# Performance work log

Hardware: AMD Instinct MI355X
Metric: run time of the kernel (lower is better)

Reference implementation:

```python
import jax, jax.numpy as jnp
import numpy as np

N_NODES = 100000
N_EDGES = 1600000
D = 128
N_LAYERS = 3
N_GRAPHS = 128


def setup_inputs() -> dict:
    key = jax.random.key(0)
    ks = jax.random.split(key, 8)
    x = jax.random.normal(ks[0], (N_NODES, D), dtype=jnp.float32)
    # stacked GIN-MLP params (all layers are D->D since hidden_dim == in_dim)
    scale = 1.0 / np.sqrt(D)
    W1 = jax.random.normal(ks[1], (N_LAYERS, D, D), dtype=jnp.float32) * scale
    b1 = jax.random.normal(ks[2], (N_LAYERS, D), dtype=jnp.float32) * 0.01
    W2 = jax.random.normal(ks[3], (N_LAYERS, D, D), dtype=jnp.float32) * scale
    b2 = jax.random.normal(ks[4], (N_LAYERS, D), dtype=jnp.float32) * 0.01
    edge_index = jax.random.randint(ks[5], (2, N_EDGES), 0, N_NODES, dtype=jnp.int64)
    batch = jnp.sort(jax.random.randint(ks[6], (N_NODES,), 0, N_GRAPHS, dtype=jnp.int64))
    return {"x": x, "W1": W1, "b1": b1, "W2": W2, "b2": b2,
            "edge_index": edge_index, "batch": batch}


def reference(x, W1, b1, W2, b2, edge_index, batch):
    src = edge_index[0]
    dst = edge_index[1]
    n = x.shape[0]
    eps = jnp.float32(0.0)  # GIN eps (PyG default, not trained)
    for i in range(N_LAYERS):
        # gather neighbor features along edges, scatter-add to destination nodes
        agg = jax.ops.segment_sum(x[src], dst, num_segments=n)  # [N, D]
        h = (1.0 + eps) * x + agg
        h = jax.nn.relu(h @ W1[i] + b1[i])
        x = h @ W2[i] + b2[i]
    # sum-pool readout per graph
    h_G = jax.ops.segment_sum(x, batch, num_segments=N_GRAPHS)  # [G, D]
    return h_G
```

## Files before the change

kernel.cpp:

```cpp
#include <hip/hip_runtime.h>
#include <hip/hip_bf16.h>
#include <stdint.h>

#define N_NODES 100000
#define N_EDGES 1600000
#define DIM 128
#define N_GRAPHS 128
#define LDA 136

#define NBKT 392
#define BCAP 6144
#define BP   5632

#define NBIN_BLK 391
#define CVT_BLK 3125

typedef unsigned int uint32;
typedef unsigned short ushort16;

typedef __bf16 bf16x8 __attribute__((ext_vector_type(8)));
typedef float fx4 __attribute__((ext_vector_type(4)));

__device__ __forceinline__ float bfLo(uint32 u){ return __builtin_bit_cast(float, (uint32)(u << 16)); }
__device__ __forceinline__ float bfHi(uint32 u){ return __builtin_bit_cast(float, (uint32)(u & 0xFFFF0000u)); }
__device__ __forceinline__ ushort16 f2bf(float f){
  uint32 u = __builtin_bit_cast(uint32, f);
  u = u + 0x7FFFu + ((u >> 16) & 1u);
  return (ushort16)(u >> 16);
}
__device__ __forceinline__ uint32 pack2(float a, float b){
  return (uint32)f2bf(a) | ((uint32)f2bf(b) << 16);
}

__global__ __launch_bounds__(512) void k_prep(const float* __restrict__ x,
                                              const float* __restrict__ W1, const float* __restrict__ W2,
                                              const int* __restrict__ ei,
                                              ushort16* __restrict__ P, ushort16* __restrict__ Q,
                                              ushort16* __restrict__ Wf,
                                              int* __restrict__ bucketCursor,
                                              int* __restrict__ temp){
  __shared__ int hist[NBKT];
  __shared__ int base[NBKT];
  __shared__ int gbase[NBKT];
  __shared__ int scanbuf[512];
  __shared__ int sVal[4096];
  __shared__ unsigned short sBkt[4096];

  int bb = blockIdx.x;
  int t  = threadIdx.x;

  if (bb < NBIN_BLK){
    int e0 = bb * 4096;
    for (int i = t; i < NBKT; i += 512) hist[i] = 0;
    __syncthreads();

    int   myv[8];
    short myb[8];
    short myr[8];
    #pragma unroll
    for (int it = 0; it < 8; ++it){
      int e = e0 + it*512 + t;
      int v = 0; short b = -1; short r = 0;
      if (e < N_EDGES){
        int s = ei[e];
        int d = ei[N_EDGES + e];
        b = (short)(d >> 8);
        v = s | ((d & 255) << 17);
        r = (short)atomicAdd(&hist[b], 1);
      }
      myv[it] = v; myb[it] = b; myr[it] = r;
    }
    __syncthreads();

    scanbuf[t] = (t < NBKT) ? hist[t] : 0;
    __syncthreads();
    for (int off = 1; off < 512; off <<= 1){
      int x2 = 0;
      if (t >= off) x2 = scanbuf[t - off];
      __syncthreads();
      scanbuf[t] += x2;
      __syncthreads();
    }
    if (t < NBKT){
      base[t]  = scanbuf[t] - hist[t];
      gbase[t] = atomicAdd(&bucketCursor[t], hist[t]);
    }
    __syncthreads();

    #pragma unroll
    for (int it = 0; it < 8; ++it){
      if (myb[it] >= 0){
        int p = base[myb[it]] + myr[it];
        sVal[p] = myv[it];
        sBkt[p] = (unsigned short)myb[it];
      }
    }
    __syncthreads();

    int cnt = scanbuf[NBKT - 1];
    for (int p = t; p < cnt; p += 512){
      int b = sBkt[p];
      int g = gbase[b] + (p - base[b]);
      if (g < BCAP) temp[b*BCAP + g] = sVal[p];
    }
    return;
  }

  if (bb < NBIN_BLK + CVT_BLK){
    int idx = ((bb - NBIN_BLK)*512 + t) * 8;
    float4 v0 = *(const float4*)(x + idx);
    float4 v1 = *(const float4*)(x + idx + 4);
    uint4 o;
    o.x = pack2(v0.x, v0.y); o.y = pack2(v0.z, v0.w);
    o.z = pack2(v1.x, v1.y); o.w = pack2(v1.z, v1.w);
    *(uint4*)(P + idx) = o;
    return;
  }

  if (bb == NBIN_BLK + CVT_BLK){
    uint4 z = {0u,0u,0u,0u};
    if (t < 16)                *(uint4*)(P + (size_t)N_NODES*128 + t*8)      = z;
    else if (t < 32)           *(uint4*)(Q + (size_t)N_NODES*128 + (t-16)*8) = z;
    return;
  }

  int tid = (bb - (NBIN_BLK + CVT_BLK + 1))*512 + t;
  int layer = tid >> 12;
  int rem   = tid & 4095;
  int mat   = rem >> 11;
  int nt    = (rem >> 8) & 7;
  int kt    = (rem >> 6) & 3;
  int lane  = rem & 63;
  int kg = lane >> 4, m = lane & 15;
  int n  = nt*16 + m;
  int kb = kt*32 + kg*8;
  const float* src = (mat ? W2 : W1) + layer*16384;
  uint4 o;
  o.x = pack2(src[(kb+0)*128 + n], src[(kb+1)*128 + n]);
  o.y = pack2(src[(kb+2)*128 + n], src[(kb+3)*128 + n]);
  o.z = pack2(src[(kb+4)*128 + n], src[(kb+5)*128 + n]);
  o.w = pack2(src[(kb+6)*128 + n], src[(kb+7)*128 + n]);
  *(uint4*)(Wf + ((((size_t)(layer*2+mat)*8 + nt)*4 + kt)*64 + lane)*8) = o;
}

__global__ __launch_bounds__(512) void k_binB(const int* __restrict__ temp,
                                              const int* __restrict__ bucketCursor,
                                              int* __restrict__ rowptr,
                                              int* __restrict__ rowlen,
                                              int* __restrict__ colx){
  __shared__ int counts[256];
  __shared__ int sc[256];
  __shared__ int cur[256];
  __shared__ int stage[BCAP];
  __shared__ int sorted[BCAP];
  int b = blockIdx.x, t = threadIdx.x;
  int cnt = min(bucketCursor[b], BCAP);
  int gb  = b * BP;
  const int* src = temp + b*BCAP;

  if (t < 256) counts[t] = 0;
  __syncthreads();
  for (int p = t; p < cnt; p += 512){
    int v = src[p];
    stage[p] = v;
    atomicAdd(&counts[v >> 17], 1);
  }
  __syncthreads();

  int len = 0, plen = 0;
  if (t < 256){
    len  = counts[t];
    plen = (len + 3) & ~3;
    sc[t] = plen;
  }
  __syncthreads();
  for (int off = 1; off < 256; off <<= 1){
    int x = 0;
    if (t < 256 && t >= off) x = sc[t - off];
    __syncthreads();
    if (t < 256) sc[t] += x;
    __syncthreads();
  }
  int excl = 0;
  if (t < 256){
    excl = sc[t] - plen;
    cur[t] = excl;
    int node = b*256 + t;
    if (node < N_NODES){ rowptr[node] = gb + excl; rowlen[node] = plen; }
  }
  __syncthreads();

  for (int p = t; p < cnt; p += 512){
    int v = stage[p];
    int d = v >> 17;
    int pos = atomicAdd(&cur[d], 1);
    sorted[pos] = v & 0x1FFFF;
  }
  __syncthreads();

  if (t < 256){
    for (int k = len; k < plen; ++k) sorted[excl + k] = N_NODES;
  }
  __syncthreads();

  int total = min(sc[255], BP);
  for (int p = t; p < total; p += 512) colx[gb + p] = sorted[p];
}

__global__ __launch_bounds__(256, 8) void k_gin(const ushort16* __restrict__ xb, ushort16* __restrict__ hb,
                                                const ushort16* __restrict__ Wt1, const float* __restrict__ b1,
                                                const ushort16* __restrict__ Wt2, const float* __restrict__ b2,
                                                const int* __restrict__ rowptr, const int* __restrict__ rowlen,
                                                const int* __restrict__ colx){
  __shared__ __attribute__((aligned(16))) ushort16 sA[64 * LDA];
  __shared__ int sOff[64];
  __shared__ int sLen[64];

  int t = threadIdx.x;
  int row0 = blockIdx.x * 64;

  if (t < 64){
    int gg = row0 + t;
    int off = 0, len = 0;
    if (gg < N_NODES){ off = rowptr[gg]; len = rowlen[gg]; }
    sOff[t] = off; sLen[t] = len;
  }
  __syncthreads();

  int wave = t >> 6, lane = t & 63;
  int g = lane >> 4, o = lane & 15;
  const uint32* xw = (const uint32*)xb;

  for (int ni = 0; ni < 16; ++ni){
    int ln  = wave*16 + ni;
    int j   = __builtin_amdgcn_readfirstlane(sOff[ln]);
    int end = j + __builtin_amdgcn_readfirstlane(sLen[ln]);

    float f0=0.f,f1=0.f,f2=0.f,f3=0.f,f4=0.f,f5=0.f,f6=0.f,f7=0.f;

    while (j + 8 <= end){
      int4 c0 = *(const int4*)(colx + j);
      int4 c1 = *(const int4*)(colx + j + 4);
      int r0ab = (g & 1) ? c0.y : c0.x;
      int r0cd = (g & 1) ? c0.w : c0.z;
      int r0   = (g & 2) ? r0cd : r0ab;
      int r1ab = (g & 1) ? c1.y : c1.x;
      int r1cd = (g & 1) ? c1.w : c1.z;
      int r1   = (g & 2) ? r1cd : r1ab;
      uint4 u0 = *(const uint4*)(xw + (size_t)r0*64 + o*4);
      uint4 u1 = *(const uint4*)(xw + (size_t)r1*64 + o*4);
      f0 += bfLo(u0.x); f1 += bfHi(u0.x); f2 += bfLo(u0.y); f3 += bfHi(u0.y);
      f4 += bfLo(u0.z); f5 += bfHi(u0.z); f6 += bfLo(u0.w); f7 += bfHi(u0.w);
      f0 += bfLo(u1.x); f1 += bfHi(u1.x); f2 += bfLo(u1.y); f3 += bfHi(u1.y);
      f4 += bfLo(u1.z); f5 += bfHi(u1.z); f6 += bfLo(u1.w); f7 += bfHi(u1.w);
      j += 8;
    }
    if (j < end){
      int4 c0 = *(const int4*)(colx + j);
      int rab = (g & 1) ? c0.y : c0.x;
      int rcd = (g & 1) ? c0.w : c0.z;
      int r0  = (g & 2) ? rcd : rab;
      uint4 u0 = *(const uint4*)(xw + (size_t)r0*64 + o*4);
      f0 += bfLo(u0.x); f1 += bfHi(u0.x); f2 += bfLo(u0.y); f3 += bfHi(u0.y);
      f4 += bfLo(u0.z); f5 += bfHi(u0.z); f6 += bfLo(u0.w); f7 += bfHi(u0.w);
    }

    f0 += __shfl_xor(f0, 16, 64); f1 += __shfl_xor(f1, 16, 64);
    f2 += __shfl_xor(f2, 16, 64); f3 += __shfl_xor(f3, 16, 64);
    f4 += __shfl_xor(f4, 16, 64); f5 += __shfl_xor(f5, 16, 64);
    f6 += __shfl_xor(f6, 16, 64); f7 += __shfl_xor(f7, 16, 64);
    f0 += __shfl_xor(f0, 32, 64); f1 += __shfl_xor(f1, 32, 64);
    f2 += __shfl_xor(f2, 32, 64); f3 += __shfl_xor(f3, 32, 64);
    f4 += __shfl_xor(f4, 32, 64); f5 += __shfl_xor(f5, 32, 64);
    f6 += __shfl_xor(f6, 32, 64); f7 += __shfl_xor(f7, 32, 64);

    if (g == 0){
      int gn = row0 + ln;
      uint4 r;
      if (gn < N_NODES){
        uint4 xv = *(const uint4*)(xw + (size_t)gn*64 + o*4);
        r.x = pack2(f0 + bfLo(xv.x), f1 + bfHi(xv.x));
        r.y = pack2(f2 + bfLo(xv.y), f3 + bfHi(xv.y));
        r.z = pack2(f4 + bfLo(xv.z), f5 + bfHi(xv.z));
        r.w = pack2(f6 + bfLo(xv.w), f7 + bfHi(xv.w));
      } else {
        r.x = r.y = r.z = r.w = 0u;
      }
      *(uint4*)(sA + ln*LDA + o*8) = r;
    }
  }
  __syncthreads();

  int m = lane & 15, kg = lane >> 4;
  int n0 = wave * 2;

  fx4 acc[4][2];
  #pragma unroll
  for (int mt = 0; mt < 4; ++mt){ acc[mt][0] = (fx4){0,0,0,0}; acc[mt][1] = (fx4){0,0,0,0}; }

  #pragma unroll
  for (int kt = 0; kt < 4; ++kt){
    bf16x8 ba = *(const bf16x8*)(Wt1 + (((n0+0)*4 + kt)*64 + lane)*8);
    bf16x8 bb = *(const bf16x8*)(Wt1 + (((n0+1)*4 + kt)*64 + lane)*8);
    #pragma unroll
    for (int mt = 0; mt < 4; ++mt){
      bf16x8 av = *(const bf16x8*)(sA + (mt*16 + m)*LDA + kg*8 + kt*32);
      acc[mt][0] = __builtin_amdgcn_mfma_f32_16x16x32_bf16(av, ba, acc[mt][0], 0, 0, 0);
      acc[mt][1] = __builtin_amdgcn_mfma_f32_16x16x32_bf16(av, bb, acc[mt][1], 0, 0, 0);
    }
  }
  float bva = b1[(n0+0)*16 + m];
  float bvb = b1[(n0+1)*16 + m];
  __syncthreads();

  #pragma unroll
  for (int mt = 0; mt < 4; ++mt){
    #pragma unroll
    for (int r = 0; r < 4; ++r){
      int row = mt*16 + kg*4 + r;
      sA[row*LDA + (n0+0)*16 + m] = f2bf(fmaxf(acc[mt][0][r] + bva, 0.f));
      sA[row*LDA + (n0+1)*16 + m] = f2bf(fmaxf(acc[mt][1][r] + bvb, 0.f));
    }
  }
  float cva = b2[(n0+0)*16 + m];
  float cvb = b2[(n0+1)*16 + m];
  #pragma unroll
  for (int mt = 0; mt < 4; ++mt){ acc[mt][0] = (fx4){0,0,0,0}; acc[mt][1] = (fx4){0,0,0,0}; }
  __syncthreads();

  #pragma unroll
  for (int kt = 0; kt < 4; ++kt){
    bf16x8 ba = *(const bf16x8*)(Wt2 + (((n0+0)*4 + kt)*64 + lane)*8);
    bf16x8 bb = *(const bf16x8*)(Wt2 + (((n0+1)*4 + kt)*64 + lane)*8);
    #pragma unroll
    for (int mt = 0; mt < 4; ++mt){
      bf16x8 av = *(const bf16x8*)(sA + (mt*16 + m)*LDA + kg*8 + kt*32);
      acc[mt][0] = __builtin_amdgcn_mfma_f32_16x16x32_bf16(av, ba, acc[mt][0], 0, 0, 0);
      acc[mt][1] = __builtin_amdgcn_mfma_f32_16x16x32_bf16(av, bb, acc[mt][1], 0, 0, 0);
    }
  }

  #pragma unroll
  for (int mt = 0; mt < 4; ++mt){
    #pragma unroll
    for (int r = 0; r < 4; ++r){
      int row = row0 + mt*16 + kg*4 + r;
      if (row < N_NODES){
        hb[row*128 + (n0+0)*16 + m] = f2bf(acc[mt][0][r] + cva);
        hb[row*128 + (n0+1)*16 + m] = f2bf(acc[mt][1][r] + cvb);
      }
    }
  }
}

__device__ __forceinline__ int lower_bound_i(const int* __restrict__ a, int n, int key){
  int lo = 0, hi = n;
  while (lo < hi){ int mid = (lo + hi) >> 1; if (a[mid] < key) lo = mid + 1; else hi = mid; }
  return lo;
}

__global__ __launch_bounds__(256) void k_pool(const ushort16* __restrict__ xb, const int* __restrict__ batch,
                                              float* __restrict__ out){
  int g = blockIdx.x >> 2;
  int p = blockIdx.x & 3;
  int start = lower_bound_i(batch, N_NODES, g);
  int end   = lower_bound_i(batch, N_NODES, g + 1);
  int t = threadIdx.x;
  int c = t & 127;
  int h = t >> 7;
  float acc = 0.f;
  for (int r = start + p*2 + h; r < end; r += 8){
    uint32 u = (uint32)xb[r*128 + c];
    acc += __builtin_bit_cast(float, (uint32)(u << 16));
  }
  __shared__ float red[256];
  red[t] = acc; __syncthreads();
  if (t < 128) atomicAdd(&out[g*128 + c], red[t] + red[t + 128]);
}

extern "C" void kernel_launch(void* const* d_in, const int* in_sizes, int n_in,
                              void* d_out, int out_size, void* d_ws, size_t ws_size,
                              hipStream_t stream) {
  const float* x   = (const float*)d_in[0];
  const float* W1  = (const float*)d_in[1];
  const float* b1  = (const float*)d_in[2];
  const float* W2  = (const float*)d_in[3];
  const float* b2  = (const float*)d_in[4];
  const int*   ei  = (const int*)d_in[5];
  const int*   bat = (const int*)d_in[6];
  float* out = (float*)d_out;

  char* w = (char*)d_ws;
  auto carve = [&](size_t bytes) -> char* {
    char* p = w; w += (bytes + 255) & ~(size_t)255; return p;
  };
  ushort16* P    = (ushort16*)carve((size_t)(N_NODES+1) * DIM * 2);
  ushort16* Q    = (ushort16*)carve((size_t)(N_NODES+1) * DIM * 2);
  ushort16* Wf   = (ushort16*)carve((size_t)3 * 2 * 16384 * 2);
  int* rowptr    = (int*)carve((size_t)N_NODES * 4);
  int* rowlen    = (int*)carve((size_t)N_NODES * 4);
  int* colx      = (int*)carve((size_t)NBKT * BP * 4);
  int* bucketCursor = (int*)carve((NBKT + 1) * 4);
  int* temp      = (int*)Q;

  hipMemsetAsync(bucketCursor, 0, (NBKT + 1) * 4, stream);
  hipMemsetAsync(d_out, 0, (size_t)N_GRAPHS * DIM * 4, stream);

  k_prep<<<NBIN_BLK + CVT_BLK + 1 + 24, 512, 0, stream>>>(x, W1, W2, ei, P, Q, Wf,
                                                          bucketCursor, temp);
  k_binB<<<NBKT, 512, 0, stream>>>(temp, bucketCursor, rowptr, rowlen, colx);

  const int ginGrid = (N_NODES + 63) / 64;

  k_gin<<<ginGrid, 256, 0, stream>>>(P, Q, Wf + 0*16384, b1 + 0*128, Wf + 1*16384, b2 + 0*128,
                                     rowptr, rowlen, colx);
  k_gin<<<ginGrid, 256, 0, stream>>>(Q, P, Wf + 2*16384, b1 + 1*128, Wf + 3*16384, b2 + 1*128,
                                     rowptr, rowlen, colx);
  k_gin<<<ginGrid, 256, 0, stream>>>(P, Q, Wf + 4*16384, b1 + 2*128, Wf + 5*16384, b2 + 2*128,
                                     rowptr, rowlen, colx);

  k_pool<<<N_GRAPHS * 4, 256, 0, stream>>>(Q, bat, out);
}
```

Baseline: 362.9 us.

## Fuse sum-pool readout into last GIN layer and use 512-thread blocks

```diff
diff --git a/kernel.cpp b/kernel.cpp
--- a/kernel.cpp
+++ b/kernel.cpp
@@ -207,23 +207,29 @@
   for (int p = t; p < total; p += 512) colx[gb + p] = sorted[p];
 }
 
-__global__ __launch_bounds__(256, 8) void k_gin(const ushort16* __restrict__ xb, ushort16* __restrict__ hb,
+template<bool LAST>
+__global__ __launch_bounds__(512, 8) void k_gin(const ushort16* __restrict__ xb, ushort16* __restrict__ hb,
                                                 const ushort16* __restrict__ Wt1, const float* __restrict__ b1,
                                                 const ushort16* __restrict__ Wt2, const float* __restrict__ b2,
                                                 const int* __restrict__ rowptr, const int* __restrict__ rowlen,
-                                                const int* __restrict__ colx){
+                                                const int* __restrict__ colx,
+                                                const int* __restrict__ batch, float* __restrict__ outp){
   __shared__ __attribute__((aligned(16))) ushort16 sA[64 * LDA];
   __shared__ int sOff[64];
   __shared__ int sLen[64];
+  __shared__ int sBat[64];
 
   int t = threadIdx.x;
   int row0 = blockIdx.x * 64;
 
   if (t < 64){
     int gg = row0 + t;
-    int off = 0, len = 0;
-    if (gg < N_NODES){ off = rowptr[gg]; len = rowlen[gg]; }
-    sOff[t] = off; sLen[t] = len;
+    int off = 0, len = 0, bg = 0;
+    if (gg < N_NODES){
+      off = rowptr[gg]; len = rowlen[gg];
+      if (LAST) bg = batch[gg];
+    }
+    sOff[t] = off; sLen[t] = len; sBat[t] = bg;
   }
   __syncthreads();
 
@@ -231,8 +237,8 @@
   int g = lane >> 4, o = lane & 15;
   const uint32* xw = (const uint32*)xb;
 
-  for (int ni = 0; ni < 16; ++ni){
-    int ln  = wave*16 + ni;
+  for (int ni = 0; ni < 8; ++ni){
+    int ln  = wave*8 + ni;
     int j   = __builtin_amdgcn_readfirstlane(sOff[ln]);
     int end = j + __builtin_amdgcn_readfirstlane(sLen[ln]);
 
@@ -292,25 +298,22 @@
   __syncthreads();
 
   int m = lane & 15, kg = lane >> 4;
-  int n0 = wave * 2;
-
-  fx4 acc[4][2];
+  int nt = wave;
+
+  fx4 acc[4];
   #pragma unroll
-  for (int mt = 0; mt < 4; ++mt){ acc[mt][0] = (fx4){0,0,0,0}; acc[mt][1] = (fx4){0,0,0,0}; }
+  for (int mt = 0; mt < 4; ++mt) acc[mt] = (fx4){0.f,0.f,0.f,0.f};
 
   #pragma unroll
   for (int kt = 0; kt < 4; ++kt){
-    bf16x8 ba = *(const bf16x8*)(Wt1 + (((n0+0)*4 + kt)*64 + lane)*8);
-    bf16x8 bb = *(const bf16x8*)(Wt1 + (((n0+1)*4 + kt)*64 + lane)*8);
+    bf16x8 ba = *(const bf16x8*)(Wt1 + ((nt*4 + kt)*64 + lane)*8);
     #pragma unroll
     for (int mt = 0; mt < 4; ++mt){
       bf16x8 av = *(const bf16x8*)(sA + (mt*16 + m)*LDA + kg*8 + kt*32);
-      acc[mt][0] = __builtin_amdgcn_mfma_f32_16x16x32_bf16(av, ba, acc[mt][0], 0, 0, 0);
-      acc[mt][1] = __builtin_amdgcn_mfma_f32_16x16x32_bf16(av, bb, acc[mt][1], 0, 0, 0);
-    }
-  }
-  float bva = b1[(n0+0)*16 + m];
-  float bvb = b1[(n0+1)*16 + m];
+      acc[mt] = __builtin_amdgcn_mfma_f32_16x16x32_bf16(av, ba, acc[mt], 0, 0, 0);
+    }
+  }
+  float bva = b1[nt*16 + m];
   __syncthreads();
 
   #pragma unroll
@@ -318,64 +321,55 @@
     #pragma unroll
     for (int r = 0; r < 4; ++r){
       int row = mt*16 + kg*4 + r;
-      sA[row*LDA + (n0+0)*16 + m] = f2bf(fmaxf(acc[mt][0][r] + bva, 0.f));
-      sA[row*LDA + (n0+1)*16 + m] = f2bf(fmaxf(acc[mt][1][r] + bvb, 0.f));
-    }
-  }
-  float cva = b2[(n0+0)*16 + m];
-  float cvb = b2[(n0+1)*16 + m];
+      sA[row*LDA + nt*16 + m] = f2bf(fmaxf(acc[mt][r] + bva, 0.f));
+    }
+  }
+  float cva = b2[nt*16 + m];
   #pragma unroll
-  for (int mt = 0; mt < 4; ++mt){ acc[mt][0] = (fx4){0,0,0,0}; acc[mt][1] = (fx4){0,0,0,0}; }
+  for (int mt = 0; mt < 4; ++mt) acc[mt] = (fx4){0.f,0.f,0.f,0.f};
   __syncthreads();
 
   #pragma unroll
   for (int kt = 0; kt < 4; ++kt){
-    bf16x8 ba = *(const bf16x8*)(Wt2 + (((n0+0)*4 + kt)*64 + lane)*8);
-    bf16x8 bb = *(const bf16x8*)(Wt2 + (((n0+1)*4 + kt)*64 + lane)*8);
+    bf16x8 ba = *(const bf16x8*)(Wt2 + ((nt*4 + kt)*64 + lane)*8);
     #pragma unroll
     for (int mt = 0; mt < 4; ++mt){
       bf16x8 av = *(const bf16x8*)(sA + (mt*16 + m)*LDA + kg*8 + kt*32);
-      acc[mt][0] = __builtin_amdgcn_mfma_f32_16x16x32_bf16(av, ba, acc[mt][0], 0, 0, 0);
-      acc[mt][1] = __builtin_amdgcn_mfma_f32_16x16x32_bf16(av, bb, acc[mt][1], 0, 0, 0);
-    }
-  }
-
-  #pragma unroll
-  for (int mt = 0; mt < 4; ++mt){
-    #pragma unroll
-    for (int r = 0; r < 4; ++r){
-      int row = row0 + mt*16 + kg*4 + r;
-      if (row < N_NODES){
-        hb[row*128 + (n0+0)*16 + m] = f2bf(acc[mt][0][r] + cva);
-        hb[row*128 + (n0+1)*16 + m] = f2bf(acc[mt][1][r] + cvb);
+      acc[mt] = __builtin_amdgcn_mfma_f32_16x16x32_bf16(av, ba, acc[mt], 0, 0, 0);
+    }
+  }
+
+  if constexpr (!LAST){
+    #pragma unroll
+    for (int mt = 0; mt < 4; ++mt){
+      #pragma unroll
+      for (int r = 0; r < 4; ++r){
+        int row = row0 + mt*16 + kg*4 + r;
+        if (row < N_NODES){
+          hb[row*128 + nt*16 + m] = f2bf(acc[mt][r] + cva);
+        }
       }
     }
-  }
-}
-
-__device__ __forceinline__ int lower_bound_i(const int* __restrict__ a, int n, int key){
-  int lo = 0, hi = n;
-  while (lo < hi){ int mid = (lo + hi) >> 1; if (a[mid] < key) lo = mid + 1; else hi = mid; }
-  return lo;
-}
-
-__global__ __launch_bounds__(256) void k_pool(const ushort16* __restrict__ xb, const int* __restrict__ batch,
-                                              float* __restrict__ out){
-  int g = blockIdx.x >> 2;
-  int p = blockIdx.x & 3;
-  int start = lower_bound_i(batch, N_NODES, g);
-  int end   = lower_bound_i(batch, N_NODES, g + 1);
-  int t = threadIdx.x;
-  int c = t & 127;
-  int h = t >> 7;
-  float acc = 0.f;
-  for (int r = start + p*2 + h; r < end; r += 8){
-    uint32 u = (uint32)xb[r*128 + c];
-    acc += __builtin_bit_cast(float, (uint32)(u << 16));
-  }
-  __shared__ float red[256];
-  red[t] = acc; __syncthreads();
-  if (t < 128) atomicAdd(&out[g*128 + c], red[t] + red[t + 128]);
+  } else {
+    float sum = 0.f; int curg = -1;
+    #pragma unroll
+    for (int mt = 0; mt < 4; ++mt){
+      #pragma unroll
+      for (int r = 0; r < 4; ++r){
+        int lrow = mt*16 + kg*4 + r;
+        int grow = row0 + lrow;
+        if (grow < N_NODES){
+          int gg = sBat[lrow];
+          if (gg != curg){
+            if (curg >= 0) atomicAdd(&outp[curg*128 + nt*16 + m], sum);
+            curg = gg; sum = 0.f;
+          }
+          sum += acc[mt][r] + cva;
+        }
+      }
+    }
+    if (curg >= 0) atomicAdd(&outp[curg*128 + nt*16 + m], sum);
+  }
 }
 
 extern "C" void kernel_launch(void* const* d_in, const int* in_sizes, int n_in,
@@ -412,12 +406,10 @@
 
   const int ginGrid = (N_NODES + 63) / 64;
 
-  k_gin<<<ginGrid, 256, 0, stream>>>(P, Q, Wf + 0*16384, b1 + 0*128, Wf + 1*16384, b2 + 0*128,
-                                     rowptr, rowlen, colx);
-  k_gin<<<ginGrid, 256, 0, stream>>>(Q, P, Wf + 2*16384, b1 + 1*128, Wf + 3*16384, b2 + 1*128,
-                                     rowptr, rowlen, colx);
-  k_gin<<<ginGrid, 256, 0, stream>>>(P, Q, Wf + 4*16384, b1 + 2*128, Wf + 5*16384, b2 + 2*128,
-                                     rowptr, rowlen, colx);
-
-  k_pool<<<N_GRAPHS * 4, 256, 0, stream>>>(Q, bat, out);
-}
+  k_gin<false><<<ginGrid, 512, 0, stream>>>(P, Q, Wf + 0*16384, b1 + 0*128, Wf + 1*16384, b2 + 0*128,
+                                            rowptr, rowlen, colx, bat, out);
+  k_gin<false><<<ginGrid, 512, 0, stream>>>(Q, P, Wf + 2*16384, b1 + 1*128, Wf + 3*16384, b2 + 1*128,
+                                            rowptr, rowlen, colx, bat, out);
+  k_gin<true><<<ginGrid, 512, 0, stream>>>(P, Q, Wf + 4*16384, b1 + 2*128, Wf + 5*16384, b2 + 2*128,
+                                           rowptr, rowlen, colx, bat, out);
+}
```

Measured after the change: 329.9 us. 1.1x faster.
